# Optimization experiments

Hardware: AMD Instinct MI355X
Metric: run time of the kernel (lower is better)

Reference implementation:

```python
import jax, jax.numpy as jnp
import numpy as np

# Four fixed 3x3 'gradient' kernels (left, right, up, down), stacked as OIHW (4,1,3,3).
_K = np.zeros((4, 1, 3, 3), np.float32)
_K[0, 0, 1, 0] = -1.0; _K[0, 0, 1, 1] = 1.0   # left:  center - left neighbor
_K[1, 0, 1, 1] = 1.0;  _K[1, 0, 1, 2] = -1.0  # right: center - right neighbor
_K[2, 0, 0, 1] = -1.0; _K[2, 0, 1, 1] = 1.0   # up:    center - upper neighbor
_K[3, 0, 1, 1] = 1.0;  _K[3, 0, 2, 1] = -1.0  # down:  center - lower neighbor
KERNELS = jnp.asarray(_K)

LOSS_WEIGHT = 1.0
POOL = 4


def _avgpool4(x):
    # AvgPool2d(4) on NCHW with H,W divisible by 4
    b, c, h, w = x.shape
    return x.reshape(b, c, h // POOL, POOL, w // POOL, POOL).mean(axis=(3, 5))


def _grad_conv(x):
    # F.conv2d(x, kernels, padding=1); x: (B,1,Hp,Wp) -> (B,4,Hp,Wp)
    return jax.lax.conv_general_dilated(
        x, KERNELS, window_strides=(1, 1), padding=((1, 1), (1, 1)),
        dimension_numbers=('NCHW', 'OIHW', 'NCHW'))


def setup_inputs() -> dict:
    key = jax.random.key(0)
    k1, k2 = jax.random.split(key)
    B, C, H, W = 32, 3, 512, 512
    x = jax.random.uniform(k1, (B, C, H, W), dtype=jnp.float32)
    pred = jax.random.uniform(k2, (B, C, H, W), dtype=jnp.float32)
    return {"x": x, "pred": pred}


def reference(x, pred):
    # channel mean -> (B,1,H,W), then 4x4 average pool -> (B,1,H/4,W/4)
    org_pool = _avgpool4(jnp.mean(x, axis=1, keepdims=True))
    enh_pool = _avgpool4(jnp.mean(pred, axis=1, keepdims=True))
    # NOTE: the original computes weight_diff and E_1 but never uses them in the
    # returned loss, so they are omitted (no effect on output or gradients).
    d = _grad_conv(org_pool) - _grad_conv(enh_pool)  # (B,4,Hp,Wp)
    # mean(D_left + D_right + D_up + D_down) == mean over (B,Hp,Wp) of channel-sum
    E = jnp.mean(jnp.sum(d * d, axis=1))
    return LOSS_WEIGHT * E
```

## Files before the change

kernel.cpp:

```cpp
#include <hip/hip_runtime.h>

constexpr int B  = 32;
constexpr int C  = 3;
constexpr int H  = 512;
constexpr int W  = 512;
constexpr int HP = H / 4;
constexpr int WP = W / 4;
constexpr int NP = B * HP * WP;

__global__ __launch_bounds__(256) void pool_diff_kernel(
        const float* __restrict__ x,
        const float* __restrict__ pred,
        float* __restrict__ p) {
    int idx = blockIdx.x * blockDim.x + threadIdx.x;
    if (idx >= NP) return;
    int px = idx & (WP - 1);
    int py = (idx >> 7) & (HP - 1);
    int b  = idx >> 14;

    size_t base = (((size_t)b * C) * H + (size_t)py * 4) * W + (size_t)px * 4;
    float s = 0.0f;
    #pragma unroll
    for (int c = 0; c < C; ++c) {
        const float4* xb = (const float4*)(x    + base + (size_t)c * H * W);
        const float4* pb = (const float4*)(pred + base + (size_t)c * H * W);
        #pragma unroll
        for (int r = 0; r < 4; ++r) {
            float4 xv = xb[r * (W / 4)];
            float4 pv = pb[r * (W / 4)];
            s += (xv.x - pv.x) + (xv.y - pv.y) + (xv.z - pv.z) + (xv.w - pv.w);
        }
    }
    p[idx] = s * (1.0f / 48.0f);
}

__global__ __launch_bounds__(256) void grad_loss_kernel(
        const float* __restrict__ p,
        float* __restrict__ out) {
    int idx = blockIdx.x * blockDim.x + threadIdx.x;
    float acc = 0.0f;
    if (idx < NP) {
        int px = idx & (WP - 1);
        int py = (idx >> 7) & (HP - 1);
        float c = p[idx];
        float l = (px > 0)      ? p[idx - 1]  : 0.0f;
        float r = (px < WP - 1) ? p[idx + 1]  : 0.0f;
        float u = (py > 0)      ? p[idx - WP] : 0.0f;
        float d = (py < HP - 1) ? p[idx + WP] : 0.0f;
        float g0 = c - l, g1 = c - r, g2 = c - u, g3 = c - d;
        acc = g0 * g0 + g1 * g1 + g2 * g2 + g3 * g3;
    }
    #pragma unroll
    for (int off = 32; off > 0; off >>= 1)
        acc += __shfl_down(acc, off, 64);

    __shared__ float ws_red[4];
    int lane = threadIdx.x & 63;
    int wid  = threadIdx.x >> 6;
    if (lane == 0) ws_red[wid] = acc;
    __syncthreads();
    if (threadIdx.x == 0) {
        float s = ws_red[0] + ws_red[1] + ws_red[2] + ws_red[3];
        atomicAdd(out, s * (1.0f / (float)NP));
    }
}

extern "C" void kernel_launch(void* const* d_in, const int* in_sizes, int n_in,
                              void* d_out, int out_size, void* d_ws, size_t ws_size,
                              hipStream_t stream) {
    const float* x    = (const float*)d_in[0];
    const float* pred = (const float*)d_in[1];
    float* out = (float*)d_out;
    float* p   = (float*)d_ws;

    hipMemsetAsync(out, 0, sizeof(float), stream);

    int threads = 256;
    int blocks  = (NP + threads - 1) / threads;
    pool_diff_kernel<<<blocks, threads, 0, stream>>>(x, pred, p);
    grad_loss_kernel<<<blocks, threads, 0, stream>>>(p, out);
}
```

Before: 240.2 us.

## Split pooling into per-plane streaming kernel plus combine pass for more parallelism

Pooling now runs one thread per (plane, pooled pixel) across all six input planes, with each thread issuing four independent float4 loads. A separate combine kernel then forms the channel-mean difference. This raises the thread count and memory-level parallelism to better saturate HBM. In exchange it writes and reads a 6xNP intermediate buffer, adds a kernel launch, and needs a larger workspace; it falls back to the old path when the workspace is too small.

```diff
diff --git a/kernel.cpp b/kernel.cpp
--- a/kernel.cpp
+++ b/kernel.cpp
@@ -7,17 +7,50 @@
 constexpr int HP = H / 4;
 constexpr int WP = W / 4;
 constexpr int NP = B * HP * WP;
+constexpr int PLANES = 6;
+
+__global__ __launch_bounds__(256) void stream_pool_kernel(
+        const float* __restrict__ x,
+        const float* __restrict__ pred,
+        float* __restrict__ q) {
+    int idx   = blockIdx.x * 256 + threadIdx.x;
+    int i     = idx & (NP - 1);
+    int plane = idx >> 19;
+    const float* src = (plane < 3) ? x : pred;
+    int c = (plane < 3) ? plane : plane - 3;
+
+    int px = i & (WP - 1);
+    int py = (i >> 7) & (HP - 1);
+    int b  = i >> 14;
+    size_t base = (((size_t)b * C + c) * H + (size_t)py * 4) * W + (size_t)px * 4;
+    const float4* sp = (const float4*)(src + base);
+
+    float4 r0 = sp[0 * (W / 4)];
+    float4 r1 = sp[1 * (W / 4)];
+    float4 r2 = sp[2 * (W / 4)];
+    float4 r3 = sp[3 * (W / 4)];
+    float s = (r0.x + r0.y + r0.z + r0.w) + (r1.x + r1.y + r1.z + r1.w)
+            + (r2.x + r2.y + r2.z + r2.w) + (r3.x + r3.y + r3.z + r3.w);
+    q[idx] = s;
+}
+
+__global__ __launch_bounds__(256) void combine_kernel(
+        const float* __restrict__ q,
+        float* __restrict__ p) {
+    int i = blockIdx.x * 256 + threadIdx.x;
+    float s = q[i] + q[i + NP] + q[i + 2 * NP]
+            - q[i + 3 * NP] - q[i + 4 * NP] - q[i + 5 * NP];
+    p[i] = s * (1.0f / 48.0f);
+}
 
 __global__ __launch_bounds__(256) void pool_diff_kernel(
         const float* __restrict__ x,
         const float* __restrict__ pred,
         float* __restrict__ p) {
     int idx = blockIdx.x * blockDim.x + threadIdx.x;
-    if (idx >= NP) return;
     int px = idx & (WP - 1);
     int py = (idx >> 7) & (HP - 1);
     int b  = idx >> 14;
-
     size_t base = (((size_t)b * C) * H + (size_t)py * 4) * W + (size_t)px * 4;
     float s = 0.0f;
     #pragma unroll
@@ -38,18 +71,16 @@
         const float* __restrict__ p,
         float* __restrict__ out) {
     int idx = blockIdx.x * blockDim.x + threadIdx.x;
-    float acc = 0.0f;
-    if (idx < NP) {
-        int px = idx & (WP - 1);
-        int py = (idx >> 7) & (HP - 1);
-        float c = p[idx];
-        float l = (px > 0)      ? p[idx - 1]  : 0.0f;
-        float r = (px < WP - 1) ? p[idx + 1]  : 0.0f;
-        float u = (py > 0)      ? p[idx - WP] : 0.0f;
-        float d = (py < HP - 1) ? p[idx + WP] : 0.0f;
-        float g0 = c - l, g1 = c - r, g2 = c - u, g3 = c - d;
-        acc = g0 * g0 + g1 * g1 + g2 * g2 + g3 * g3;
-    }
+    int px = idx & (WP - 1);
+    int py = (idx >> 7) & (HP - 1);
+    float c = p[idx];
+    float l = (px > 0)      ? p[idx - 1]  : 0.0f;
+    float r = (px < WP - 1) ? p[idx + 1]  : 0.0f;
+    float u = (py > 0)      ? p[idx - WP] : 0.0f;
+    float d = (py < HP - 1) ? p[idx + WP] : 0.0f;
+    float g0 = c - l, g1 = c - r, g2 = c - u, g3 = c - d;
+    float acc = g0 * g0 + g1 * g1 + g2 * g2 + g3 * g3;
+
     #pragma unroll
     for (int off = 32; off > 0; off >>= 1)
         acc += __shfl_down(acc, off, 64);
@@ -71,12 +102,19 @@
     const float* x    = (const float*)d_in[0];
     const float* pred = (const float*)d_in[1];
     float* out = (float*)d_out;
-    float* p   = (float*)d_ws;
 
     hipMemsetAsync(out, 0, sizeof(float), stream);
 
-    int threads = 256;
-    int blocks  = (NP + threads - 1) / threads;
-    pool_diff_kernel<<<blocks, threads, 0, stream>>>(x, pred, p);
-    grad_loss_kernel<<<blocks, threads, 0, stream>>>(p, out);
+    const size_t need = (size_t)(PLANES + 1) * NP * sizeof(float);
+    if (ws_size >= need) {
+        float* q = (float*)d_ws;
+        float* p = q + (size_t)PLANES * NP;
+        stream_pool_kernel<<<PLANES * NP / 256, 256, 0, stream>>>(x, pred, q);
+        combine_kernel<<<NP / 256, 256, 0, stream>>>(q, p);
+        grad_loss_kernel<<<NP / 256, 256, 0, stream>>>(p, out);
+    } else {
+        float* p = (float*)d_ws;
+        pool_diff_kernel<<<NP / 256, 256, 0, stream>>>(x, pred, p);
+        grad_loss_kernel<<<NP / 256, 256, 0, stream>>>(p, out);
+    }
 }
```

Measured after the change: 245.7 us. +2.3%, slower.

## Fuse pooling and gradient loss into one tiled kernel with shared-memory halo

Applied to the files above, without the earlier changes.

Merges the pooling-difference kernel and the gradient-loss kernel into a single kernel. Each block computes a 34x34 pooled tile including halo into shared memory, then evaluates the four directional differences from LDS. This removes the intermediate pooled buffer and the second launch. In exchange, halo cells are recomputed and the grid shrinks to 512 blocks, which reduces memory-level parallelism.

```diff
diff --git a/kernel.cpp b/kernel.cpp
--- a/kernel.cpp
+++ b/kernel.cpp
@@ -8,58 +8,73 @@
 constexpr int WP = W / 4;
 constexpr int NP = B * HP * WP;
 
-__global__ __launch_bounds__(256) void pool_diff_kernel(
+constexpr int TS = 32;
+constexpr int HS = TS + 2;
+constexpr int TILES_PER_IMG = (HP / TS) * (WP / TS);
+constexpr int NBLOCKS = B * TILES_PER_IMG;
+
+__global__ __launch_bounds__(256) void spatial_loss_fused(
         const float* __restrict__ x,
         const float* __restrict__ pred,
-        float* __restrict__ p) {
-    int idx = blockIdx.x * blockDim.x + threadIdx.x;
-    if (idx >= NP) return;
-    int px = idx & (WP - 1);
-    int py = (idx >> 7) & (HP - 1);
-    int b  = idx >> 14;
+        float* __restrict__ out) {
+    __shared__ float pt[HS][HS + 1];
 
-    size_t base = (((size_t)b * C) * H + (size_t)py * 4) * W + (size_t)px * 4;
-    float s = 0.0f;
+    int blk = blockIdx.x;
+    int b   = blk >> 4;
+    int ty  = (blk >> 2) & 3;
+    int tx  = blk & 3;
+    int tid = threadIdx.x;
+
+    for (int i = tid; i < HS * HS; i += 256) {
+        int hy = i / HS;
+        int hx = i - hy * HS;
+        int gy = ty * TS + hy - 1;
+        int gx = tx * TS + hx - 1;
+        float s = 0.0f;
+        if ((unsigned)gy < (unsigned)HP && (unsigned)gx < (unsigned)WP) {
+            size_t base = (((size_t)b * C) * H + (size_t)gy * 4) * W + (size_t)gx * 4;
+            #pragma unroll
+            for (int c = 0; c < C; ++c) {
+                const float4* xb = (const float4*)(x    + base + (size_t)c * H * W);
+                const float4* pb = (const float4*)(pred + base + (size_t)c * H * W);
+                #pragma unroll
+                for (int r = 0; r < 4; ++r) {
+                    float4 xv = xb[r * (W / 4)];
+                    float4 pv = pb[r * (W / 4)];
+                    s += (xv.x - pv.x) + (xv.y - pv.y) + (xv.z - pv.z) + (xv.w - pv.w);
+                }
+            }
+            s *= (1.0f / 48.0f);
+        }
+        pt[hy][hx] = s;
+    }
+    __syncthreads();
+
+    float acc = 0.0f;
     #pragma unroll
-    for (int c = 0; c < C; ++c) {
-        const float4* xb = (const float4*)(x    + base + (size_t)c * H * W);
-        const float4* pb = (const float4*)(pred + base + (size_t)c * H * W);
-        #pragma unroll
-        for (int r = 0; r < 4; ++r) {
-            float4 xv = xb[r * (W / 4)];
-            float4 pv = pb[r * (W / 4)];
-            s += (xv.x - pv.x) + (xv.y - pv.y) + (xv.z - pv.z) + (xv.w - pv.w);
-        }
+    for (int j = 0; j < (TS * TS) / 256; ++j) {
+        int i  = tid + j * 256;
+        int iy = i >> 5;
+        int ix = i & 31;
+        float c = pt[iy + 1][ix + 1];
+        float l = pt[iy + 1][ix + 0];
+        float r = pt[iy + 1][ix + 2];
+        float u = pt[iy + 0][ix + 1];
+        float d = pt[iy + 2][ix + 1];
+        float g0 = c - l, g1 = c - r, g2 = c - u, g3 = c - d;
+        acc += g0 * g0 + g1 * g1 + g2 * g2 + g3 * g3;
     }
-    p[idx] = s * (1.0f / 48.0f);
-}
 
-__global__ __launch_bounds__(256) void grad_loss_kernel(
-        const float* __restrict__ p,
-        float* __restrict__ out) {
-    int idx = blockIdx.x * blockDim.x + threadIdx.x;
-    float acc = 0.0f;
-    if (idx < NP) {
-        int px = idx & (WP - 1);
-        int py = (idx >> 7) & (HP - 1);
-        float c = p[idx];
-        float l = (px > 0)      ? p[idx - 1]  : 0.0f;
-        float r = (px < WP - 1) ? p[idx + 1]  : 0.0f;
-        float u = (py > 0)      ? p[idx - WP] : 0.0f;
-        float d = (py < HP - 1) ? p[idx + WP] : 0.0f;
-        float g0 = c - l, g1 = c - r, g2 = c - u, g3 = c - d;
-        acc = g0 * g0 + g1 * g1 + g2 * g2 + g3 * g3;
-    }
     #pragma unroll
     for (int off = 32; off > 0; off >>= 1)
         acc += __shfl_down(acc, off, 64);
 
     __shared__ float ws_red[4];
-    int lane = threadIdx.x & 63;
-    int wid  = threadIdx.x >> 6;
+    int lane = tid & 63;
+    int wid  = tid >> 6;
     if (lane == 0) ws_red[wid] = acc;
     __syncthreads();
-    if (threadIdx.x == 0) {
+    if (tid == 0) {
         float s = ws_red[0] + ws_red[1] + ws_red[2] + ws_red[3];
         atomicAdd(out, s * (1.0f / (float)NP));
     }
@@ -71,12 +86,8 @@
     const float* x    = (const float*)d_in[0];
     const float* pred = (const float*)d_in[1];
     float* out = (float*)d_out;
-    float* p   = (float*)d_ws;
 
     hipMemsetAsync(out, 0, sizeof(float), stream);
 
-    int threads = 256;
-    int blocks  = (NP + threads - 1) / threads;
-    pool_diff_kernel<<<blocks, threads, 0, stream>>>(x, pred, p);
-    grad_loss_kernel<<<blocks, threads, 0, stream>>>(p, out);
+    spatial_loss_fused<<<NBLOCKS, 256, 0, stream>>>(x, pred, out);
 }
```

Result: faster. 220.7 us (-8.1%).
